# Kernel tuning notes

Measured on AMD Instinct MI355X. Metric: run time of the kernel, lower is better.

The kernel has to match this reference:

```python
import jax, jax.numpy as jnp
import numpy as np
from jax import lax

EPS = 1e-5
DN = ('NCHW', 'OIHW', 'NCHW')

@jax.custom_vjp
def binact(x):
    # XNOR-Net BinActive: sign forward, STE backward (grad zeroed where |x|>1)
    return jnp.sign(x)

def _binact_fwd(x):
    return jnp.sign(x), x

def _binact_bwd(x, g):
    return (g * (jnp.abs(x) <= 1).astype(g.dtype),)

binact.defvjp(_binact_fwd, _binact_bwd)

def bn(x, gamma, beta, mean, var):
    scale = gamma * lax.rsqrt(var + EPS)
    return x * scale[None, :, None, None] + (beta - mean * scale)[None, :, None, None]

def conv(x, w, stride=1, pad=0):
    return lax.conv_general_dilated(x, w, (stride, stride), [(pad, pad), (pad, pad)],
                                    dimension_numbers=DN)

def setup_inputs() -> dict:
    key = jax.random.key(0)
    ks = jax.random.split(key, 16)
    inplanes, planes = 1024, 256
    d = {}
    d['x'] = jax.random.normal(ks[0], (64, inplanes, 14, 14), jnp.float32)
    d['bn1_gamma'] = jax.random.uniform(ks[1], (inplanes,), jnp.float32)
    d['bn1_beta'] = jax.random.normal(ks[2], (inplanes,), jnp.float32)
    d['bn1_mean'] = jax.random.normal(ks[3], (inplanes,), jnp.float32)
    d['bn1_var'] = jax.random.uniform(ks[4], (inplanes,), jnp.float32)
    d['W1'] = jax.random.normal(ks[5], (planes, inplanes, 1, 1), jnp.float32) * 0.05
    d['bn2_gamma'] = jax.random.uniform(ks[6], (planes,), jnp.float32)
    d['bn2_beta'] = jax.random.normal(ks[7], (planes,), jnp.float32)
    d['bn2_mean'] = jax.random.normal(ks[8], (planes,), jnp.float32)
    d['bn2_var'] = jax.random.uniform(ks[9], (planes,), jnp.float32)
    d['W2'] = jax.random.normal(ks[10], (planes, planes, 3, 3), jnp.float32) * 0.05
    d['bn3_gamma'] = jax.random.uniform(ks[11], (planes,), jnp.float32)
    d['bn3_beta'] = jax.random.normal(ks[12], (planes,), jnp.float32)
    d['bn3_mean'] = jax.random.normal(ks[13], (planes,), jnp.float32)
    d['bn3_var'] = jax.random.uniform(ks[14], (planes,), jnp.float32)
    d['W3'] = jax.random.normal(ks[15], (planes * 4, planes, 1, 1), jnp.float32) * 0.05
    return d

def reference(x, bn1_gamma, bn1_beta, bn1_mean, bn1_var, W1,
              bn2_gamma, bn2_beta, bn2_mean, bn2_var, W2,
              bn3_gamma, bn3_beta, bn3_mean, bn3_var, W3):
    residual = x
    h = binact(bn(x, bn1_gamma, bn1_beta, bn1_mean, bn1_var))
    h = jax.nn.relu(conv(h, W1))                      # 1x1
    h = binact(bn(h, bn2_gamma, bn2_beta, bn2_mean, bn2_var))
    h = jax.nn.relu(conv(h, W2, stride=1, pad=1))     # 3x3
    h = binact(bn(h, bn3_gamma, bn3_beta, bn3_mean, bn3_var))
    h = conv(h, W3)                                   # 1x1 expansion
    return jax.nn.relu(h + residual)
```

## Files before the change

### kernel.cpp

```cpp
#include <hip/hip_runtime.h>

#define EPS 1e-5f

typedef __attribute__((ext_vector_type(8))) short bf16x8;
typedef __attribute__((ext_vector_type(4))) float f32x4;

#define MFMA16(a, b, c) __builtin_amdgcn_mfma_f32_16x16x32_bf16(a, b, c, 0, 0, 0)

__device__ __forceinline__ void gl16(const void* g, void* l) {
    __builtin_amdgcn_global_load_lds(
        (const __attribute__((address_space(1))) unsigned int*)g,
        (__attribute__((address_space(3))) unsigned int*)l, 16, 0, 0);
}

__device__ __forceinline__ unsigned short f2bf(float f) {
    unsigned u = __float_as_uint(f);
    unsigned r = (u + 0x7FFFu + ((u >> 16) & 1u)) >> 16;
    return (unsigned short)r;
}
__device__ __forceinline__ float bf2f(unsigned short h) {
    return __uint_as_float(((unsigned)h) << 16);
}


__global__ __launch_bounds__(256) void k_prep(
    const float* __restrict__ W1, const float* __restrict__ W2,
    const float* __restrict__ W3,
    unsigned short* __restrict__ A1, unsigned short* __restrict__ A2,
    unsigned short* __restrict__ A3)
{
    int i = blockIdx.x * 256 + threadIdx.x;
    if (i < 262144) {
        float w = W1[i];
        unsigned short h1 = f2bf(w); float r1 = w - bf2f(h1);
        unsigned short h2 = f2bf(r1); float r2 = r1 - bf2f(h2);
        unsigned short h3 = f2bf(r2);
        A1[i] = h1; A1[262144 + i] = h2; A1[524288 + i] = h3;
        A3[i] = f2bf(W3[i]);
    }
    if (i < 589824) {
        int co = i / 2304, k = i - co * 2304;
        int ci = k / 9, tap = k - ci * 9;
        int o = co * 2304 + tap * 256 + ci;
        float w = W2[i];
        unsigned short h1 = f2bf(w); float r1 = w - bf2f(h1);
        unsigned short h2 = f2bf(r1); float r2 = r1 - bf2f(h2);
        unsigned short h3 = f2bf(r2);
        A2[o] = h1; A2[589824 + o] = h2; A2[1179648 + o] = h3;
    }
}

__global__ __launch_bounds__(256, 2) void k_act1(
    const float* __restrict__ x,
    const float* __restrict__ g, const float* __restrict__ b,
    const float* __restrict__ mm, const float* __restrict__ vv,
    unsigned short* __restrict__ b1)
{
    __shared__ unsigned short tile[128 * 197];
    __shared__ float ssc[128], ssh[128];
    const int tid = threadIdx.x;
    const int n = blockIdx.x, c0 = blockIdx.y * 128;
    if (tid < 128) {
        int c = c0 + tid;
        float sc = g[c] * (1.0f / sqrtf(vv[c] + EPS));
        ssc[tid] = sc;
        ssh[tid] = b[c] - mm[c] * sc;
    }
    __syncthreads();
    const float* xp = x + ((size_t)n * 1024 + c0) * 196;
    for (int it = 0; it < 98; ++it) {
        int e = it * 256 + tid;
        int c = e / 196, p = e - c * 196;
        float t = xp[e] * ssc[c] + ssh[c];
        tile[c * 197 + p] = (t > 0.f) ? 0x3F80 : ((t < 0.f) ? 0xBF80 : 0);
    }
    __syncthreads();
    const int pr = tid >> 4, cg = (tid & 15) * 8;
    for (int it = 0; it < 13; ++it) {
        int p = it * 16 + pr;
        if (p < 196) {
            unsigned short vals[8];
            #pragma unroll
            for (int j = 0; j < 8; ++j) vals[j] = tile[(cg + j) * 197 + p];
            uint4 pk;
            pk.x = (unsigned)vals[0] | ((unsigned)vals[1] << 16);
            pk.y = (unsigned)vals[2] | ((unsigned)vals[3] << 16);
            pk.z = (unsigned)vals[4] | ((unsigned)vals[5] << 16);
            pk.w = (unsigned)vals[6] | ((unsigned)vals[7] << 16);
            *(uint4*)&b1[((size_t)n * 196 + p) * 1024 + c0 + cg] = pk;
        }
    }
}

__global__ __launch_bounds__(256) void k_zb(unsigned short* __restrict__ b2p) {
    int t = blockIdx.x * 256 + threadIdx.x;
    if (t >= 122880) return;
    int ci8 = t & 31;
    int tb = t >> 5;
    int bidx = tb % 60, n = tb / 60;
    int sp;
    if (bidx < 16) sp = bidx;
    else if (bidx < 32) sp = 240 + (bidx - 16);
    else { int s2 = bidx - 32; sp = ((s2 >> 1) + 1) * 16 + (s2 & 1) * 15; }
    ulonglong2 z; z.x = 0; z.y = 0;
    *(ulonglong2*)&b2p[((size_t)(n * 256 + sp)) * 256 + ci8 * 8] = z;
}

__global__ __launch_bounds__(256, 2) void k_gemm1(
    const unsigned short* __restrict__ A1, const unsigned short* __restrict__ B1,
    const float* __restrict__ g2, const float* __restrict__ be2,
    const float* __restrict__ mu2, const float* __restrict__ va2,
    unsigned short* __restrict__ b2p)
{
    __shared__ unsigned short sA[3][2048];
    __shared__ unsigned short sB[4096];
    const int tid = threadIdx.x;
    const int co0 = blockIdx.x * 64;
    const int m0  = blockIdx.y * 128;
    const int lane = tid & 63, w = tid >> 6;
    const int wr = w & 1, wc = w >> 1;
    const int srow = tid >> 2;
    const int sq = (tid & 3) ^ ((tid >> 3) & 3);
    const int frow = lane & 15;
    const int fq = (lane >> 4) ^ ((frow >> 1) & 3);

    const unsigned short* gA = A1 + (size_t)(co0 + srow) * 1024 + sq * 8;
    const unsigned short* gB0 = B1 + (size_t)(m0 + srow) * 1024 + sq * 8;
    const unsigned short* gB1 = B1 + (size_t)(m0 + 64 + srow) * 1024 + sq * 8;

    f32x4 acc[2][4];
    #pragma unroll
    for (int i = 0; i < 2; ++i)
        #pragma unroll
        for (int j = 0; j < 4; ++j) acc[i][j] = (f32x4){0.f, 0.f, 0.f, 0.f};

    for (int k0 = 0; k0 < 1024; k0 += 32) {
        gl16(gA + k0,            &sA[0][tid * 8]);
        gl16(gA + 262144 + k0,   &sA[1][tid * 8]);
        gl16(gA + 524288 + k0,   &sA[2][tid * 8]);
        gl16(gB0 + k0, &sB[tid * 8]);
        gl16(gB1 + k0, &sB[(256 + tid) * 8]);
        __syncthreads();
        bf16x8 af[3][2], bfr[4];
        #pragma unroll
        for (int s = 0; s < 3; ++s)
            #pragma unroll
            for (int fr = 0; fr < 2; ++fr)
                af[s][fr] = *(const bf16x8*)&sA[s][(wr * 32 + fr * 16 + frow) * 32 + fq * 8];
        #pragma unroll
        for (int fc = 0; fc < 4; ++fc)
            bfr[fc] = *(const bf16x8*)&sB[(wc * 64 + fc * 16 + frow) * 32 + fq * 8];
        #pragma unroll
        for (int s = 0; s < 3; ++s)
            #pragma unroll
            for (int fr = 0; fr < 2; ++fr)
                #pragma unroll
                for (int fc = 0; fc < 4; ++fc)
                    acc[fr][fc] = MFMA16(af[s][fr], bfr[fc], acc[fr][fc]);
        __syncthreads();
    }
    #pragma unroll
    for (int fc = 0; fc < 4; ++fc) {
        int m = m0 + wc * 64 + fc * 16 + frow;
        int n = m / 196, p = m - n * 196;
        int y = p / 14, xx = p - y * 14;
        size_t ob = ((size_t)(n * 256 + (y + 1) * 16 + (xx + 1))) * 256;
        #pragma unroll
        for (int fr = 0; fr < 2; ++fr) {
            int co = co0 + wr * 32 + fr * 16 + (lane >> 4) * 4;
            unsigned short o[4];
            #pragma unroll
            for (int r = 0; r < 4; ++r) {
                float sc = g2[co + r] * (1.0f / sqrtf(va2[co + r] + EPS));
                float sh = be2[co + r] - mu2[co + r] * sc;
                float h = fmaxf(acc[fr][fc][r], 0.f);
                float t = h * sc + sh;
                o[r] = (t > 0.f) ? 0x3F80 : ((t < 0.f) ? 0xBF80 : 0);
            }
            ushort4 pk; pk.x = o[0]; pk.y = o[1]; pk.z = o[2]; pk.w = o[3];
            *(ushort4*)&b2p[ob + co] = pk;
        }
    }
}

__global__ __launch_bounds__(256, 2) void k_gemm2(
    const unsigned short* __restrict__ A2, const unsigned short* __restrict__ b2p,
    const float* __restrict__ g3, const float* __restrict__ be3,
    const float* __restrict__ mu3, const float* __restrict__ va3,
    unsigned short* __restrict__ b3)
{
    __shared__ unsigned short sA[3][2048];
    __shared__ unsigned short sB[4096];
    const int tid = threadIdx.x;
    const int co0 = blockIdx.x * 64;
    const int m0  = blockIdx.y * 128;
    const int nB  = m0 >> 8;
    const int sp0 = m0 & 255;
    const int lane = tid & 63, w = tid >> 6;
    const int wr = w & 1, wc = w >> 1;
    const int srow = tid >> 2;
    const int sq = (tid & 3) ^ ((tid >> 3) & 3);
    const int frow = lane & 15;
    const int fq = (lane >> 4) ^ ((frow >> 1) & 3);

    const long bbase = (long)(nB * 256 + sp0) * 256;

    f32x4 acc[2][4];
    #pragma unroll
    for (int i = 0; i < 2; ++i)
        #pragma unroll
        for (int j = 0; j < 4; ++j) acc[i][j] = (f32x4){0.f, 0.f, 0.f, 0.f};

    for (int tap = 0; tap < 9; ++tap) {
        int dy = tap / 3, dx = tap - dy * 3;
        int toff = (dy - 1) * 16 + (dx - 1);
        const unsigned short* gA = A2 + (size_t)(co0 + srow) * 2304 + tap * 256 + sq * 8;
        const long brow0 = bbase + (long)toff * 256 + (long)srow * 256 + sq * 8;
        for (int ci0 = 0; ci0 < 256; ci0 += 32) {
            gl16(gA + ci0,           &sA[0][tid * 8]);
            gl16(gA + 589824 + ci0,  &sA[1][tid * 8]);
            gl16(gA + 1179648 + ci0, &sA[2][tid * 8]);
            gl16(b2p + brow0 + ci0,             &sB[tid * 8]);
            gl16(b2p + brow0 + 64 * 256 + ci0,  &sB[(256 + tid) * 8]);
            __syncthreads();
            bf16x8 af[3][2], bfr[4];
            #pragma unroll
            for (int s = 0; s < 3; ++s)
                #pragma unroll
                for (int fr = 0; fr < 2; ++fr)
                    af[s][fr] = *(const bf16x8*)&sA[s][(wr * 32 + fr * 16 + frow) * 32 + fq * 8];
            #pragma unroll
            for (int fc = 0; fc < 4; ++fc)
                bfr[fc] = *(const bf16x8*)&sB[(wc * 64 + fc * 16 + frow) * 32 + fq * 8];
            #pragma unroll
            for (int s = 0; s < 3; ++s)
                #pragma unroll
                for (int fr = 0; fr < 2; ++fr)
                    #pragma unroll
                    for (int fc = 0; fc < 4; ++fc)
                        acc[fr][fc] = MFMA16(af[s][fr], bfr[fc], acc[fr][fc]);
            __syncthreads();
        }
    }
    #pragma unroll
    for (int fc = 0; fc < 4; ++fc) {
        int m = m0 + wc * 64 + fc * 16 + frow;
        int sp = m & 255, nn = m >> 8;
        int y = sp >> 4, xx = sp & 15;
        if (y >= 1 && y <= 14 && xx >= 1 && xx <= 14) {
            int p = (y - 1) * 14 + (xx - 1);
            size_t ob = ((size_t)nn * 196 + p) * 256;
            #pragma unroll
            for (int fr = 0; fr < 2; ++fr) {
                int co = co0 + wr * 32 + fr * 16 + (lane >> 4) * 4;
                unsigned short o[4];
                #pragma unroll
                for (int r = 0; r < 4; ++r) {
                    float sc = g3[co + r] * (1.0f / sqrtf(va3[co + r] + EPS));
                    float sh = be3[co + r] - mu3[co + r] * sc;
                    float h = fmaxf(acc[fr][fc][r], 0.f);
                    float t = h * sc + sh;
                    o[r] = (t > 0.f) ? 0x3F80 : ((t < 0.f) ? 0xBF80 : 0);
                }
                ushort4 pk; pk.x = o[0]; pk.y = o[1]; pk.z = o[2]; pk.w = o[3];
                *(ushort4*)&b3[ob + co] = pk;
            }
        }
    }
}

__global__ __launch_bounds__(256, 2) void k_gemm3(
    const unsigned short* __restrict__ A3, const unsigned short* __restrict__ B3,
    const float* __restrict__ xres, float* __restrict__ out)
{
    __shared__ unsigned short sA[4096];
    __shared__ unsigned short sB[4096];
    const int tid = threadIdx.x;
    const int co0 = blockIdx.x * 128;
    const int m0  = blockIdx.y * 128;
    const int lane = tid & 63, w = tid >> 6;
    const int wr = w >> 1, wc = w & 1;
    const int srow = tid >> 2;
    const int sq = (tid & 3) ^ ((tid >> 3) & 3);
    const int frow = lane & 15;
    const int fq = (lane >> 4) ^ ((frow >> 1) & 3);

    f32x4 acc[4][4];
    #pragma unroll
    for (int i = 0; i < 4; ++i)
        #pragma unroll
        for (int j = 0; j < 4; ++j) acc[i][j] = (f32x4){0.f, 0.f, 0.f, 0.f};

    for (int k0 = 0; k0 < 256; k0 += 32) {
        gl16(A3 + (size_t)(co0 + srow) * 256 + k0 + sq * 8,      &sA[tid * 8]);
        gl16(A3 + (size_t)(co0 + 64 + srow) * 256 + k0 + sq * 8, &sA[(256 + tid) * 8]);
        gl16(B3 + (size_t)(m0 + srow) * 256 + k0 + sq * 8,       &sB[tid * 8]);
        gl16(B3 + (size_t)(m0 + 64 + srow) * 256 + k0 + sq * 8,  &sB[(256 + tid) * 8]);
        __syncthreads();
        bf16x8 af[4], bfr[4];
        #pragma unroll
        for (int fr = 0; fr < 4; ++fr)
            af[fr] = *(const bf16x8*)&sA[(wr * 64 + fr * 16 + frow) * 32 + fq * 8];
        #pragma unroll
        for (int fc = 0; fc < 4; ++fc)
            bfr[fc] = *(const bf16x8*)&sB[(wc * 64 + fc * 16 + frow) * 32 + fq * 8];
        #pragma unroll
        for (int fr = 0; fr < 4; ++fr)
            #pragma unroll
            for (int fc = 0; fc < 4; ++fc)
                acc[fr][fc] = MFMA16(af[fr], bfr[fc], acc[fr][fc]);
        __syncthreads();
    }
    #pragma unroll
    for (int fc = 0; fc < 4; ++fc) {
        int m = m0 + wc * 64 + fc * 16 + frow;
        int n = m / 196, p = m - n * 196;
        #pragma unroll
        for (int fr = 0; fr < 4; ++fr) {
            int co = co0 + wr * 64 + fr * 16 + (lane >> 4) * 4;
            size_t idx = ((size_t)n * 1024 + co) * 196 + p;
            #pragma unroll
            for (int r = 0; r < 4; ++r)
                out[idx + (size_t)r * 196] =
                    fmaxf(acc[fr][fc][r] + xres[idx + (size_t)r * 196], 0.f);
        }
    }
}

extern "C" void kernel_launch(void* const* d_in, const int* in_sizes, int n_in,
                              void* d_out, int out_size, void* d_ws, size_t ws_size,
                              hipStream_t stream) {
    const float* x   = (const float*)d_in[0];
    const float* g1  = (const float*)d_in[1];
    const float* be1 = (const float*)d_in[2];
    const float* mu1 = (const float*)d_in[3];
    const float* va1 = (const float*)d_in[4];
    const float* W1  = (const float*)d_in[5];
    const float* g2  = (const float*)d_in[6];
    const float* be2 = (const float*)d_in[7];
    const float* mu2 = (const float*)d_in[8];
    const float* va2 = (const float*)d_in[9];
    const float* W2  = (const float*)d_in[10];
    const float* g3  = (const float*)d_in[11];
    const float* be3 = (const float*)d_in[12];
    const float* mu3 = (const float*)d_in[13];
    const float* va3 = (const float*)d_in[14];
    const float* W3  = (const float*)d_in[15];
    float* out = (float*)d_out;

    char* p = (char*)d_ws;
    unsigned short* A1 = (unsigned short*)p;            p += 3 * 262144 * 2;
    unsigned short* A2 = (unsigned short*)p;            p += 3 * 589824 * 2;
    unsigned short* A3 = (unsigned short*)p;            p += 262144 * 2;
    unsigned short* b1 = (unsigned short*)p;            p += (size_t)12544 * 1024 * 2;
    p += 16384;
    unsigned short* b2p = (unsigned short*)p;           p += (size_t)64 * 256 * 256 * 2;
    p += 16384;
    unsigned short* b3 = (unsigned short*)p;

    k_prep<<<2304, 256, 0, stream>>>(W1, W2, W3, A1, A2, A3);
    k_act1<<<dim3(64, 8), 256, 0, stream>>>(x, g1, be1, mu1, va1, b1);
    k_zb<<<480, 256, 0, stream>>>(b2p);
    k_gemm1<<<dim3(4, 98), 256, 0, stream>>>(A1, b1, g2, be2, mu2, va2, b2p);
    k_gemm2<<<dim3(4, 128), 256, 0, stream>>>(A2, b2p, g3, be3, mu3, va3, b3);
    k_gemm3<<<dim3(8, 98), 256, 0, stream>>>(A3, b3, x, out);
}
```

Measured before the change: 290.6 us.

## Merge prep kernels, double-buffer GEMM LDS stages, remap blocks, precompute BN scales

```diff
diff --git a/kernel.cpp b/kernel.cpp
--- a/kernel.cpp
+++ b/kernel.cpp
@@ -23,100 +23,123 @@
 }
 
 
-__global__ __launch_bounds__(256) void k_prep(
-    const float* __restrict__ W1, const float* __restrict__ W2,
+__global__ __launch_bounds__(256, 2) void k_pre(
+    const float* __restrict__ x,
+    const float* __restrict__ g1, const float* __restrict__ be1,
+    const float* __restrict__ mu1, const float* __restrict__ va1,
+    const float* __restrict__ W1,
+    const float* __restrict__ g2, const float* __restrict__ be2,
+    const float* __restrict__ mu2, const float* __restrict__ va2,
+    const float* __restrict__ W2,
+    const float* __restrict__ g3, const float* __restrict__ be3,
+    const float* __restrict__ mu3, const float* __restrict__ va3,
     const float* __restrict__ W3,
     unsigned short* __restrict__ A1, unsigned short* __restrict__ A2,
-    unsigned short* __restrict__ A3)
-{
-    int i = blockIdx.x * 256 + threadIdx.x;
-    if (i < 262144) {
-        float w = W1[i];
-        unsigned short h1 = f2bf(w); float r1 = w - bf2f(h1);
-        unsigned short h2 = f2bf(r1); float r2 = r1 - bf2f(h2);
-        unsigned short h3 = f2bf(r2);
-        A1[i] = h1; A1[262144 + i] = h2; A1[524288 + i] = h3;
-        A3[i] = f2bf(W3[i]);
-    }
-    if (i < 589824) {
-        int co = i / 2304, k = i - co * 2304;
-        int ci = k / 9, tap = k - ci * 9;
-        int o = co * 2304 + tap * 256 + ci;
-        float w = W2[i];
-        unsigned short h1 = f2bf(w); float r1 = w - bf2f(h1);
-        unsigned short h2 = f2bf(r1); float r2 = r1 - bf2f(h2);
-        unsigned short h3 = f2bf(r2);
-        A2[o] = h1; A2[589824 + o] = h2; A2[1179648 + o] = h3;
-    }
-}
-
-__global__ __launch_bounds__(256, 2) void k_act1(
-    const float* __restrict__ x,
-    const float* __restrict__ g, const float* __restrict__ b,
-    const float* __restrict__ mm, const float* __restrict__ vv,
-    unsigned short* __restrict__ b1)
+    unsigned short* __restrict__ A3,
+    float* __restrict__ sc2, float* __restrict__ sh2,
+    float* __restrict__ sc3, float* __restrict__ sh3,
+    unsigned short* __restrict__ b1, unsigned short* __restrict__ b2p)
 {
     __shared__ unsigned short tile[128 * 197];
     __shared__ float ssc[128], ssh[128];
+    const int wg = blockIdx.x;
     const int tid = threadIdx.x;
-    const int n = blockIdx.x, c0 = blockIdx.y * 128;
-    if (tid < 128) {
-        int c = c0 + tid;
-        float sc = g[c] * (1.0f / sqrtf(vv[c] + EPS));
-        ssc[tid] = sc;
-        ssh[tid] = b[c] - mm[c] * sc;
-    }
-    __syncthreads();
-    const float* xp = x + ((size_t)n * 1024 + c0) * 196;
-    for (int it = 0; it < 98; ++it) {
-        int e = it * 256 + tid;
-        int c = e / 196, p = e - c * 196;
-        float t = xp[e] * ssc[c] + ssh[c];
-        tile[c * 197 + p] = (t > 0.f) ? 0x3F80 : ((t < 0.f) ? 0xBF80 : 0);
-    }
-    __syncthreads();
-    const int pr = tid >> 4, cg = (tid & 15) * 8;
-    for (int it = 0; it < 13; ++it) {
-        int p = it * 16 + pr;
-        if (p < 196) {
-            unsigned short vals[8];
-            #pragma unroll
-            for (int j = 0; j < 8; ++j) vals[j] = tile[(cg + j) * 197 + p];
-            uint4 pk;
-            pk.x = (unsigned)vals[0] | ((unsigned)vals[1] << 16);
-            pk.y = (unsigned)vals[2] | ((unsigned)vals[3] << 16);
-            pk.z = (unsigned)vals[4] | ((unsigned)vals[5] << 16);
-            pk.w = (unsigned)vals[6] | ((unsigned)vals[7] << 16);
-            *(uint4*)&b1[((size_t)n * 196 + p) * 1024 + c0 + cg] = pk;
-        }
-    }
-}
-
-__global__ __launch_bounds__(256) void k_zb(unsigned short* __restrict__ b2p) {
-    int t = blockIdx.x * 256 + threadIdx.x;
-    if (t >= 122880) return;
-    int ci8 = t & 31;
-    int tb = t >> 5;
-    int bidx = tb % 60, n = tb / 60;
-    int sp;
-    if (bidx < 16) sp = bidx;
-    else if (bidx < 32) sp = 240 + (bidx - 16);
-    else { int s2 = bidx - 32; sp = ((s2 >> 1) + 1) * 16 + (s2 & 1) * 15; }
-    ulonglong2 z; z.x = 0; z.y = 0;
-    *(ulonglong2*)&b2p[((size_t)(n * 256 + sp)) * 256 + ci8 * 8] = z;
+
+    if (wg < 512) {
+        const int n = wg >> 3, c0 = (wg & 7) * 128;
+        if (tid < 128) {
+            int c = c0 + tid;
+            float sc = g1[c] * (1.0f / sqrtf(va1[c] + EPS));
+            ssc[tid] = sc;
+            ssh[tid] = be1[c] - mu1[c] * sc;
+        }
+        __syncthreads();
+        const float4* xp4 = (const float4*)(x + ((size_t)n * 1024 + c0) * 196);
+        for (int it = 0; it < 25; ++it) {
+            int e = it * 256 + tid;
+            if (e < 6272) {
+                int c = e / 49, q = e - c * 49, p = q * 4;
+                float4 xv = xp4[e];
+                float sc = ssc[c], sh = ssh[c];
+                float t0 = xv.x * sc + sh, t1 = xv.y * sc + sh;
+                float t2 = xv.z * sc + sh, t3 = xv.w * sc + sh;
+                unsigned short* tp = &tile[c * 197 + p];
+                tp[0] = (t0 > 0.f) ? 0x3F80 : ((t0 < 0.f) ? 0xBF80 : 0);
+                tp[1] = (t1 > 0.f) ? 0x3F80 : ((t1 < 0.f) ? 0xBF80 : 0);
+                tp[2] = (t2 > 0.f) ? 0x3F80 : ((t2 < 0.f) ? 0xBF80 : 0);
+                tp[3] = (t3 > 0.f) ? 0x3F80 : ((t3 < 0.f) ? 0xBF80 : 0);
+            }
+        }
+        __syncthreads();
+        const int pr = tid >> 4, cg = (tid & 15) * 8;
+        for (int it = 0; it < 13; ++it) {
+            int p = it * 16 + pr;
+            if (p < 196) {
+                unsigned short vals[8];
+                #pragma unroll
+                for (int j = 0; j < 8; ++j) vals[j] = tile[(cg + j) * 197 + p];
+                uint4 pk;
+                pk.x = (unsigned)vals[0] | ((unsigned)vals[1] << 16);
+                pk.y = (unsigned)vals[2] | ((unsigned)vals[3] << 16);
+                pk.z = (unsigned)vals[4] | ((unsigned)vals[5] << 16);
+                pk.w = (unsigned)vals[6] | ((unsigned)vals[7] << 16);
+                *(uint4*)&b1[((size_t)n * 196 + p) * 1024 + c0 + cg] = pk;
+            }
+        }
+    } else if (wg < 2816) {
+        int i = (wg - 512) * 256 + tid;
+        if (i < 262144) {
+            float w = W1[i];
+            unsigned short h1 = f2bf(w); float r1 = w - bf2f(h1);
+            unsigned short h2 = f2bf(r1); float r2 = r1 - bf2f(h2);
+            unsigned short h3 = f2bf(r2);
+            A1[i] = h1; A1[262144 + i] = h2; A1[524288 + i] = h3;
+            A3[i] = f2bf(W3[i]);
+        }
+        {
+            int co = i / 2304, k = i - co * 2304;
+            int ci = k / 9, tap = k - ci * 9;
+            int o = co * 2304 + tap * 256 + ci;
+            float w = W2[i];
+            unsigned short h1 = f2bf(w); float r1 = w - bf2f(h1);
+            unsigned short h2 = f2bf(r1); float r2 = r1 - bf2f(h2);
+            unsigned short h3 = f2bf(r2);
+            A2[o] = h1; A2[589824 + o] = h2; A2[1179648 + o] = h3;
+        }
+        if (i < 256) {
+            float s2 = g2[i] * (1.0f / sqrtf(va2[i] + EPS));
+            sc2[i] = s2; sh2[i] = be2[i] - mu2[i] * s2;
+            float s3 = g3[i] * (1.0f / sqrtf(va3[i] + EPS));
+            sc3[i] = s3; sh3[i] = be3[i] - mu3[i] * s3;
+        }
+    } else {
+        int t = (wg - 2816) * 256 + tid;
+        if (t < 122880) {
+            int ci8 = t & 31;
+            int tb = t >> 5;
+            int bidx = tb % 60, n = tb / 60;
+            int sp;
+            if (bidx < 16) sp = bidx;
+            else if (bidx < 32) sp = 240 + (bidx - 16);
+            else { int s2 = bidx - 32; sp = ((s2 >> 1) + 1) * 16 + (s2 & 1) * 15; }
+            ulonglong2 z; z.x = 0; z.y = 0;
+            *(ulonglong2*)&b2p[((size_t)(n * 256 + sp)) * 256 + ci8 * 8] = z;
+        }
+    }
 }
 
 __global__ __launch_bounds__(256, 2) void k_gemm1(
     const unsigned short* __restrict__ A1, const unsigned short* __restrict__ B1,
-    const float* __restrict__ g2, const float* __restrict__ be2,
-    const float* __restrict__ mu2, const float* __restrict__ va2,
+    const float* __restrict__ sc2, const float* __restrict__ sh2,
     unsigned short* __restrict__ b2p)
 {
-    __shared__ unsigned short sA[3][2048];
-    __shared__ unsigned short sB[4096];
+    __shared__ unsigned short sA[2][3][2048];
+    __shared__ unsigned short sB[2][4096];
     const int tid = threadIdx.x;
-    const int co0 = blockIdx.x * 64;
-    const int m0  = blockIdx.y * 128;
+    const int wg = blockIdx.x;
+    const int r = (wg & 7) * 49 + (wg >> 3);
+    const int co0 = (r & 3) * 64;
+    const int m0  = (r >> 2) * 128;
     const int lane = tid & 63, w = tid >> 6;
     const int wr = w & 1, wc = w >> 1;
     const int srow = tid >> 2;
@@ -124,32 +147,39 @@
     const int frow = lane & 15;
     const int fq = (lane >> 4) ^ ((frow >> 1) & 3);
 
-    const unsigned short* gA = A1 + (size_t)(co0 + srow) * 1024 + sq * 8;
+    const unsigned short* gA  = A1 + (size_t)(co0 + srow) * 1024 + sq * 8;
     const unsigned short* gB0 = B1 + (size_t)(m0 + srow) * 1024 + sq * 8;
     const unsigned short* gB1 = B1 + (size_t)(m0 + 64 + srow) * 1024 + sq * 8;
 
+    auto STAGE = [&](int t, int c) {
+        int k0 = t << 5;
+        gl16(gA + k0,          &sA[c][0][tid * 8]);
+        gl16(gA + 262144 + k0, &sA[c][1][tid * 8]);
+        gl16(gA + 524288 + k0, &sA[c][2][tid * 8]);
+        gl16(gB0 + k0, &sB[c][tid * 8]);
+        gl16(gB1 + k0, &sB[c][2048 + tid * 8]);
+    };
+
     f32x4 acc[2][4];
     #pragma unroll
     for (int i = 0; i < 2; ++i)
         #pragma unroll
         for (int j = 0; j < 4; ++j) acc[i][j] = (f32x4){0.f, 0.f, 0.f, 0.f};
 
-    for (int k0 = 0; k0 < 1024; k0 += 32) {
-        gl16(gA + k0,            &sA[0][tid * 8]);
-        gl16(gA + 262144 + k0,   &sA[1][tid * 8]);
-        gl16(gA + 524288 + k0,   &sA[2][tid * 8]);
-        gl16(gB0 + k0, &sB[tid * 8]);
-        gl16(gB1 + k0, &sB[(256 + tid) * 8]);
-        __syncthreads();
+    STAGE(0, 0);
+    __syncthreads();
+    int cur = 0;
+    for (int t = 0; t < 32; ++t) {
+        if (t < 31) STAGE(t + 1, cur ^ 1);
         bf16x8 af[3][2], bfr[4];
         #pragma unroll
         for (int s = 0; s < 3; ++s)
             #pragma unroll
             for (int fr = 0; fr < 2; ++fr)
-                af[s][fr] = *(const bf16x8*)&sA[s][(wr * 32 + fr * 16 + frow) * 32 + fq * 8];
+                af[s][fr] = *(const bf16x8*)&sA[cur][s][(wr * 32 + fr * 16 + frow) * 32 + fq * 8];
         #pragma unroll
         for (int fc = 0; fc < 4; ++fc)
-            bfr[fc] = *(const bf16x8*)&sB[(wc * 64 + fc * 16 + frow) * 32 + fq * 8];
+            bfr[fc] = *(const bf16x8*)&sB[cur][(wc * 64 + fc * 16 + frow) * 32 + fq * 8];
         #pragma unroll
         for (int s = 0; s < 3; ++s)
             #pragma unroll
@@ -158,6 +188,7 @@
                 for (int fc = 0; fc < 4; ++fc)
                     acc[fr][fc] = MFMA16(af[s][fr], bfr[fc], acc[fr][fc]);
         __syncthreads();
+        cur ^= 1;
     }
     #pragma unroll
     for (int fc = 0; fc < 4; ++fc) {
@@ -170,12 +201,10 @@
             int co = co0 + wr * 32 + fr * 16 + (lane >> 4) * 4;
             unsigned short o[4];
             #pragma unroll
-            for (int r = 0; r < 4; ++r) {
-                float sc = g2[co + r] * (1.0f / sqrtf(va2[co + r] + EPS));
-                float sh = be2[co + r] - mu2[co + r] * sc;
-                float h = fmaxf(acc[fr][fc][r], 0.f);
-                float t = h * sc + sh;
-                o[r] = (t > 0.f) ? 0x3F80 : ((t < 0.f) ? 0xBF80 : 0);
+            for (int q = 0; q < 4; ++q) {
+                float h = fmaxf(acc[fr][fc][q], 0.f);
+                float t = h * sc2[co + q] + sh2[co + q];
+                o[q] = (t > 0.f) ? 0x3F80 : ((t < 0.f) ? 0xBF80 : 0);
             }
             ushort4 pk; pk.x = o[0]; pk.y = o[1]; pk.z = o[2]; pk.w = o[3];
             *(ushort4*)&b2p[ob + co] = pk;
@@ -185,15 +214,16 @@
 
 __global__ __launch_bounds__(256, 2) void k_gemm2(
     const unsigned short* __restrict__ A2, const unsigned short* __restrict__ b2p,
-    const float* __restrict__ g3, const float* __restrict__ be3,
-    const float* __restrict__ mu3, const float* __restrict__ va3,
+    const float* __restrict__ sc3, const float* __restrict__ sh3,
     unsigned short* __restrict__ b3)
 {
-    __shared__ unsigned short sA[3][2048];
-    __shared__ unsigned short sB[4096];
+    __shared__ unsigned short sA[2][3][2048];
+    __shared__ unsigned short sB[2][4096];
     const int tid = threadIdx.x;
-    const int co0 = blockIdx.x * 64;
-    const int m0  = blockIdx.y * 128;
+    const int wg = blockIdx.x;
+    const int r = (wg & 7) * 64 + (wg >> 3);
+    const int co0 = (r & 3) * 64;
+    const int m0  = (r >> 2) * 128;
     const int nB  = m0 >> 8;
     const int sp0 = m0 & 255;
     const int lane = tid & 63, w = tid >> 6;
@@ -205,42 +235,48 @@
 
     const long bbase = (long)(nB * 256 + sp0) * 256;
 
+    auto STAGE = [&](int t, int c) {
+        int tap = t >> 3, ci0 = (t & 7) << 5;
+        int dy = (tap * 11) >> 5, dx = tap - dy * 3;
+        int toff = (dy - 1) * 16 + dx - 1;
+        const unsigned short* gA = A2 + (size_t)(co0 + srow) * 2304 + tap * 256 + ci0 + sq * 8;
+        gl16(gA,           &sA[c][0][tid * 8]);
+        gl16(gA + 589824,  &sA[c][1][tid * 8]);
+        gl16(gA + 1179648, &sA[c][2][tid * 8]);
+        long boff = bbase + (long)(toff + srow) * 256 + ci0 + sq * 8;
+        gl16(b2p + boff,             &sB[c][tid * 8]);
+        gl16(b2p + boff + 64 * 256,  &sB[c][2048 + tid * 8]);
+    };
+
     f32x4 acc[2][4];
     #pragma unroll
     for (int i = 0; i < 2; ++i)
         #pragma unroll
         for (int j = 0; j < 4; ++j) acc[i][j] = (f32x4){0.f, 0.f, 0.f, 0.f};
 
-    for (int tap = 0; tap < 9; ++tap) {
-        int dy = tap / 3, dx = tap - dy * 3;
-        int toff = (dy - 1) * 16 + (dx - 1);
-        const unsigned short* gA = A2 + (size_t)(co0 + srow) * 2304 + tap * 256 + sq * 8;
-        const long brow0 = bbase + (long)toff * 256 + (long)srow * 256 + sq * 8;
-        for (int ci0 = 0; ci0 < 256; ci0 += 32) {
-            gl16(gA + ci0,           &sA[0][tid * 8]);
-            gl16(gA + 589824 + ci0,  &sA[1][tid * 8]);
-            gl16(gA + 1179648 + ci0, &sA[2][tid * 8]);
-            gl16(b2p + brow0 + ci0,             &sB[tid * 8]);
-            gl16(b2p + brow0 + 64 * 256 + ci0,  &sB[(256 + tid) * 8]);
-            __syncthreads();
-            bf16x8 af[3][2], bfr[4];
-            #pragma unroll
-            for (int s = 0; s < 3; ++s)
+    STAGE(0, 0);
+    __syncthreads();
+    int cur = 0;
+    for (int t = 0; t < 72; ++t) {
+        if (t < 71) STAGE(t + 1, cur ^ 1);
+        bf16x8 af[3][2], bfr[4];
+        #pragma unroll
+        for (int s = 0; s < 3; ++s)
+            #pragma unroll
+            for (int fr = 0; fr < 2; ++fr)
+                af[s][fr] = *(const bf16x8*)&sA[cur][s][(wr * 32 + fr * 16 + frow) * 32 + fq * 8];
+        #pragma unroll
+        for (int fc = 0; fc < 4; ++fc)
+            bfr[fc] = *(const bf16x8*)&sB[cur][(wc * 64 + fc * 16 + frow) * 32 + fq * 8];
+        #pragma unroll
+        for (int s = 0; s < 3; ++s)
+            #pragma unroll
+            for (int fr = 0; fr < 2; ++fr)
                 #pragma unroll
-                for (int fr = 0; fr < 2; ++fr)
-                    af[s][fr] = *(const bf16x8*)&sA[s][(wr * 32 + fr * 16 + frow) * 32 + fq * 8];
-            #pragma unroll
-            for (int fc = 0; fc < 4; ++fc)
-                bfr[fc] = *(const bf16x8*)&sB[(wc * 64 + fc * 16 + frow) * 32 + fq * 8];
-            #pragma unroll
-            for (int s = 0; s < 3; ++s)
-                #pragma unroll
-                for (int fr = 0; fr < 2; ++fr)
-                    #pragma unroll
-                    for (int fc = 0; fc < 4; ++fc)
-                        acc[fr][fc] = MFMA16(af[s][fr], bfr[fc], acc[fr][fc]);
-            __syncthreads();
-        }
+                for (int fc = 0; fc < 4; ++fc)
+                    acc[fr][fc] = MFMA16(af[s][fr], bfr[fc], acc[fr][fc]);
+        __syncthreads();
+        cur ^= 1;
     }
     #pragma unroll
     for (int fc = 0; fc < 4; ++fc) {
@@ -255,12 +291,10 @@
                 int co = co0 + wr * 32 + fr * 16 + (lane >> 4) * 4;
                 unsigned short o[4];
                 #pragma unroll
-                for (int r = 0; r < 4; ++r) {
-                    float sc = g3[co + r] * (1.0f / sqrtf(va3[co + r] + EPS));
-                    float sh = be3[co + r] - mu3[co + r] * sc;
-                    float h = fmaxf(acc[fr][fc][r], 0.f);
-                    float t = h * sc + sh;
-                    o[r] = (t > 0.f) ? 0x3F80 : ((t < 0.f) ? 0xBF80 : 0);
+                for (int q = 0; q < 4; ++q) {
+                    float h = fmaxf(acc[fr][fc][q], 0.f);
+                    float t = h * sc3[co + q] + sh3[co + q];
+                    o[q] = (t > 0.f) ? 0x3F80 : ((t < 0.f) ? 0xBF80 : 0);
                 }
                 ushort4 pk; pk.x = o[0]; pk.y = o[1]; pk.z = o[2]; pk.w = o[3];
                 *(ushort4*)&b3[ob + co] = pk;
@@ -269,15 +303,17 @@
     }
 }
 
-__global__ __launch_bounds__(256, 2) void k_gemm3(
+__global__ __launch_bounds__(256, 3) void k_gemm3(
     const unsigned short* __restrict__ A3, const unsigned short* __restrict__ B3,
     const float* __restrict__ xres, float* __restrict__ out)
 {
-    __shared__ unsigned short sA[4096];
-    __shared__ unsigned short sB[4096];
+    __shared__ unsigned short sA[2][4096];
+    __shared__ unsigned short sB[2][4096];
     const int tid = threadIdx.x;
-    const int co0 = blockIdx.x * 128;
-    const int m0  = blockIdx.y * 128;
+    const int wg = blockIdx.x;
+    const int r = (wg & 7) * 98 + (wg >> 3);
+    const int co0 = (r & 7) * 128;
+    const int m0  = (r >> 3) * 128;
     const int lane = tid & 63, w = tid >> 6;
     const int wr = w >> 1, wc = w & 1;
     const int srow = tid >> 2;
@@ -285,31 +321,39 @@
     const int frow = lane & 15;
     const int fq = (lane >> 4) ^ ((frow >> 1) & 3);
 
+    auto STAGE = [&](int t, int c) {
+        int k0 = t << 5;
+        gl16(A3 + (size_t)(co0 + srow) * 256 + k0 + sq * 8,      &sA[c][tid * 8]);
+        gl16(A3 + (size_t)(co0 + 64 + srow) * 256 + k0 + sq * 8, &sA[c][2048 + tid * 8]);
+        gl16(B3 + (size_t)(m0 + srow) * 256 + k0 + sq * 8,       &sB[c][tid * 8]);
+        gl16(B3 + (size_t)(m0 + 64 + srow) * 256 + k0 + sq * 8,  &sB[c][2048 + tid * 8]);
+    };
+
     f32x4 acc[4][4];
     #pragma unroll
     for (int i = 0; i < 4; ++i)
         #pragma unroll
         for (int j = 0; j < 4; ++j) acc[i][j] = (f32x4){0.f, 0.f, 0.f, 0.f};
 
-    for (int k0 = 0; k0 < 256; k0 += 32) {
-        gl16(A3 + (size_t)(co0 + srow) * 256 + k0 + sq * 8,      &sA[tid * 8]);
-        gl16(A3 + (size_t)(co0 + 64 + srow) * 256 + k0 + sq * 8, &sA[(256 + tid) * 8]);
-        gl16(B3 + (size_t)(m0 + srow) * 256 + k0 + sq * 8,       &sB[tid * 8]);
-        gl16(B3 + (size_t)(m0 + 64 + srow) * 256 + k0 + sq * 8,  &sB[(256 + tid) * 8]);
-        __syncthreads();
+    STAGE(0, 0);
+    __syncthreads();
+    int cur = 0;
+    for (int t = 0; t < 8; ++t) {
+        if (t < 7) STAGE(t + 1, cur ^ 1);
         bf16x8 af[4], bfr[4];
         #pragma unroll
         for (int fr = 0; fr < 4; ++fr)
-            af[fr] = *(const bf16x8*)&sA[(wr * 64 + fr * 16 + frow) * 32 + fq * 8];
+            af[fr] = *(const bf16x8*)&sA[cur][(wr * 64 + fr * 16 + frow) * 32 + fq * 8];
         #pragma unroll
         for (int fc = 0; fc < 4; ++fc)
-            bfr[fc] = *(const bf16x8*)&sB[(wc * 64 + fc * 16 + frow) * 32 + fq * 8];
+            bfr[fc] = *(const bf16x8*)&sB[cur][(wc * 64 + fc * 16 + frow) * 32 + fq * 8];
         #pragma unroll
         for (int fr = 0; fr < 4; ++fr)
             #pragma unroll
             for (int fc = 0; fc < 4; ++fc)
                 acc[fr][fc] = MFMA16(af[fr], bfr[fc], acc[fr][fc]);
         __syncthreads();
+        cur ^= 1;
     }
     #pragma unroll
     for (int fc = 0; fc < 4; ++fc) {
@@ -320,9 +364,9 @@
             int co = co0 + wr * 64 + fr * 16 + (lane >> 4) * 4;
             size_t idx = ((size_t)n * 1024 + co) * 196 + p;
             #pragma unroll
-            for (int r = 0; r < 4; ++r)
-                out[idx + (size_t)r * 196] =
-                    fmaxf(acc[fr][fc][r] + xres[idx + (size_t)r * 196], 0.f);
+            for (int q = 0; q < 4; ++q)
+                out[idx + (size_t)q * 196] =
+                    fmaxf(acc[fr][fc][q] + xres[idx + (size_t)q * 196], 0.f);
         }
     }
 }
@@ -349,19 +393,24 @@
     float* out = (float*)d_out;
 
     char* p = (char*)d_ws;
-    unsigned short* A1 = (unsigned short*)p;            p += 3 * 262144 * 2;
-    unsigned short* A2 = (unsigned short*)p;            p += 3 * 589824 * 2;
-    unsigned short* A3 = (unsigned short*)p;            p += 262144 * 2;
-    unsigned short* b1 = (unsigned short*)p;            p += (size_t)12544 * 1024 * 2;
+    unsigned short* A1 = (unsigned short*)p;  p += 3 * 262144 * 2;
+    unsigned short* A2 = (unsigned short*)p;  p += 3 * 589824 * 2;
+    unsigned short* A3 = (unsigned short*)p;  p += 262144 * 2;
+    float* sc2 = (float*)p;                   p += 256 * 4;
+    float* sh2 = (float*)p;                   p += 256 * 4;
+    float* sc3 = (float*)p;                   p += 256 * 4;
+    float* sh3 = (float*)p;                   p += 256 * 4;
+    unsigned short* b1 = (unsigned short*)p;  p += (size_t)12544 * 1024 * 2;
     p += 16384;
-    unsigned short* b2p = (unsigned short*)p;           p += (size_t)64 * 256 * 256 * 2;
+    unsigned short* b2p = (unsigned short*)p; p += (size_t)64 * 256 * 256 * 2;
     p += 16384;
     unsigned short* b3 = (unsigned short*)p;
 
-    k_prep<<<2304, 256, 0, stream>>>(W1, W2, W3, A1, A2, A3);
-    k_act1<<<dim3(64, 8), 256, 0, stream>>>(x, g1, be1, mu1, va1, b1);
-    k_zb<<<480, 256, 0, stream>>>(b2p);
-    k_gemm1<<<dim3(4, 98), 256, 0, stream>>>(A1, b1, g2, be2, mu2, va2, b2p);
-    k_gemm2<<<dim3(4, 128), 256, 0, stream>>>(A2, b2p, g3, be3, mu3, va3, b3);
-    k_gemm3<<<dim3(8, 98), 256, 0, stream>>>(A3, b3, x, out);
-}
+    k_pre<<<3296, 256, 0, stream>>>(x, g1, be1, mu1, va1, W1,
+                                    g2, be2, mu2, va2, W2,
+                                    g3, be3, mu3, va3, W3,
+                                    A1, A2, A3, sc2, sh2, sc3, sh3, b1, b2p);
+    k_gemm1<<<392, 256, 0, stream>>>(A1, b1, sc2, sh2, b2p);
+    k_gemm2<<<512, 256, 0, stream>>>(A2, b2p, sc3, sh3, b3);
+    k_gemm3<<<784, 256, 0, stream>>>(A3, b3, x, out);
+}
```

Measured after the change: 267.1 us. 1.09x faster.
